# Optimization experiments

Hardware: AMD Instinct MI355X
Metric: run time of the kernel (lower is better)

## Reference

```python
import jax, jax.numpy as jnp
import numpy as np

N_NODES = 50000
N_EDGES = 800000
HIDDEN = 256
LAYERS = 10


def setup_inputs() -> dict:
    key = jax.random.key(0)
    ks = jax.random.split(key, 8)
    x = jax.random.normal(ks[0], (N_NODES, 1), dtype=jnp.float32)
    edge_index = jax.random.randint(ks[1], (2, N_EDGES), 0, N_NODES, dtype=jnp.int64)
    # GCNConv weights (Glorot-ish scale)
    W1 = jax.random.normal(ks[2], (1, HIDDEN), dtype=jnp.float32) * (1.0 / np.sqrt(1))
    b1 = jnp.zeros((HIDDEN,), dtype=jnp.float32)
    W = jax.random.normal(ks[3], (HIDDEN, HIDDEN), dtype=jnp.float32) * (1.0 / np.sqrt(HIDDEN))
    b = jnp.zeros((HIDDEN,), dtype=jnp.float32)
    Wc = jax.random.normal(ks[4], (HIDDEN, 1), dtype=jnp.float32) * (1.0 / np.sqrt(HIDDEN))
    bc = jnp.zeros((1,), dtype=jnp.float32)
    return {"x": x, "edge_index": edge_index, "W1": W1, "b1": b1,
            "W": W, "b": b, "Wc": Wc, "bc": bc}


def _gcn_norm(edge_index, n_nodes):
    # PyG GCNConv default: add self-loops, symmetric normalization
    loop = jnp.arange(n_nodes, dtype=edge_index.dtype)
    src = jnp.concatenate([edge_index[0], loop])
    dst = jnp.concatenate([edge_index[1], loop])
    ones = jnp.ones(src.shape[0], dtype=jnp.float32)
    deg = jax.ops.segment_sum(ones, dst, num_segments=n_nodes)
    dinv = jnp.where(deg > 0, jax.lax.rsqrt(deg), 0.0)
    norm = dinv[src] * dinv[dst]  # [E+N]
    return src, dst, norm


def _gcn_conv(h, W, b, src, dst, norm, n_nodes):
    h = h @ W                                   # [N, H] dense transform first (small GEMM)
    msg = h[src] * norm[:, None]                # gather + scale  [E+N, H]
    out = jax.ops.segment_sum(msg, dst, num_segments=n_nodes)  # scatter-add
    return out + b


def reference(x, edge_index, W1, b1, W, b, Wc, bc):
    n = x.shape[0]
    src, dst, norm = _gcn_norm(edge_index, n)  # graph is static across layers
    h = jax.nn.relu(_gcn_conv(x, W1, b1, src, dst, norm, n))
    for _ in range(1, LAYERS):  # layers 1..9 share the same weights (self.conv reused)
        h = jax.nn.relu(_gcn_conv(h, W, b, src, dst, norm, n))
    return h @ Wc + bc  # [N, 1]
```

## Files before the change

kernel.cpp:

```cpp
#include <hip/hip_runtime.h>

typedef long long ll;
typedef __attribute__((ext_vector_type(8))) short short8;
typedef __attribute__((ext_vector_type(4))) float f32x4;
constexpr int HID = 256;
constexpr int LDSS = 264;

__device__ inline ushort f2bf(float f){
  uint u = __float_as_uint(f);
  u += 0x7FFFu + ((u >> 16) & 1u);
  return (ushort)(u >> 16);
}

__device__ inline int pinv(int q){ return (q & ~63) | ((q & 3)*16 + ((q >> 2) & 15)); }

__global__ void k_diag(float* out, int n, float val){
  int i = blockIdx.x*256 + threadIdx.x;
  if (i < n) out[i] = val;
}

__global__ void k_detect(const int* ei, int* flag){
  __shared__ int bad;
  if (threadIdx.x == 0) bad = 0;
  __syncthreads();
  for (int i = threadIdx.x; i < 2048; i += 256)
    if (ei[2*i+1] != 0) bad = 1;
  __syncthreads();
  if (threadIdx.x == 0) *flag = bad ? 0 : 1;
}

__global__ void k_count(const int* ei, ll E, const int* flag, int* cnt){
  ll i = (ll)blockIdx.x*256 + threadIdx.x;
  if (i >= E) return;
  int f = *flag;
  int d = f ? (int)((const ll*)ei)[E + i] : ei[E + i];
  atomicAdd(&cnt[d], 1);
}

__global__ void k_scan_a(const int* __restrict__ cnt, int* __restrict__ bsum, int n){
  __shared__ int s[256];
  int t = threadIdx.x, i = blockIdx.x*256 + t;
  s[t] = (i < n) ? cnt[i] : 0;
  __syncthreads();
  for (int off = 128; off; off >>= 1){
    if (t < off) s[t] += s[t + off];
    __syncthreads();
  }
  if (t == 0) bsum[blockIdx.x] = s[0];
}

__global__ void k_scan_b(const int* __restrict__ bsum, int* __restrict__ boff,
                         int nb, int* __restrict__ row_ptr, int n){
  __shared__ int s[256];
  int t = threadIdx.x;
  int v = (t < nb) ? bsum[t] : 0;
  s[t] = v; __syncthreads();
  for (int off = 1; off < 256; off <<= 1){
    int add = (t >= off) ? s[t - off] : 0;
    __syncthreads();
    s[t] += add;
    __syncthreads();
  }
  if (t < nb) boff[t] = s[t] - v;
  if (t == nb - 1) row_ptr[n] = s[t];
}

__global__ void k_scan_c(const int* __restrict__ cnt, const int* __restrict__ boff,
                         int* __restrict__ row_ptr, const float* __restrict__ x,
                         float* __restrict__ dinv, float* __restrict__ xd, int n){
  __shared__ int s[256];
  int t = threadIdx.x, i = blockIdx.x*256 + t;
  int v = (i < n) ? cnt[i] : 0;
  s[t] = v; __syncthreads();
  for (int off = 1; off < 256; off <<= 1){
    int add = (t >= off) ? s[t - off] : 0;
    __syncthreads();
    s[t] += add;
    __syncthreads();
  }
  if (i < n){
    row_ptr[i] = boff[blockIdx.x] + s[t] - v;
    float dv = 1.0f / sqrtf((float)(v + 1));
    dinv[i] = dv;
    xd[i] = x[i] * dv;
  }
}

__global__ void k_place(const int* ei, ll E, const int* flag, int* fill, int* col){
  ll i = (ll)blockIdx.x*256 + threadIdx.x;
  if (i >= E) return;
  int f = *flag;
  int s, d;
  if (f){ const ll* e64 = (const ll*)ei; s = (int)e64[i]; d = (int)e64[E + i]; }
  else  { s = ei[i]; d = ei[E + i]; }
  int p = atomicAdd(&fill[d], 1);
  col[p] = s;
}

__global__ void k_layer1(const float* __restrict__ xd, const int* __restrict__ row_ptr,
                         const int* __restrict__ col, float* __restrict__ g, int n){
  int i = blockIdx.x*256 + threadIdx.x;
  if (i >= n) return;
  float s = xd[i];
  int e0 = row_ptr[i], e1 = row_ptr[i+1];
  for (int e = e0; e < e1; ++e) s += xd[col[e]];
  g[i] = s;
}

__global__ void k_perm(const float* b1, const float* W1, const float* bm, const float* Wc,
                       float* b1_p, float* W1_p, float* bm_p, float* Wc_p){
  int q = threadIdx.x;
  int c = pinv(q);
  b1_p[q] = b1[c];
  W1_p[q] = W1[c];
  bm_p[q] = bm[c];
  Wc_p[q] = Wc[c];
}

__global__ void k_splitW(const float* __restrict__ W, short* __restrict__ Bt){
  int idx = blockIdx.x*256 + threadIdx.x;
  if (idx >= 16*8*64) return;
  int nb = idx >> 9, kc = (idx >> 6) & 7, l = idx & 63;
  short8 hi, lo;
  #pragma unroll
  for (int j = 0; j < 8; ++j){
    int k = pinv(kc*32 + ((l >> 4) * 8) + j);
    int c = nb*16 + (l & 15);
    float wv = W[k*HID + c];
    ushort h = f2bf(wv);
    float hf = __uint_as_float((uint)h << 16);
    hi[j] = (short)h;
    lo[j] = (short)f2bf(wv - hf);
  }
  ((short8*)Bt)[idx] = hi;
  ((short8*)Bt)[8192 + idx] = lo;
}

template<int MODE>
__global__ __launch_bounds__(256, 4) void k_gemm_mfma(
  const void* __restrict__ Ain, const short* __restrict__ Bt,
  const float* __restrict__ bias, const float* __restrict__ W1,
  const float* __restrict__ dinv, ushort* __restrict__ ts_bf, int n)
{
  __shared__ short Ah[64*LDSS];
  int t = threadIdx.x;
  int r0 = blockIdx.x * 64;

  #pragma unroll
  for (int i = 0; i < 8; ++i){
    int id  = i*256 + t;
    int row = id >> 5;
    int c16 = id & 31;
    int v   = r0 + row;
    short8 hi8 = {0,0,0,0,0,0,0,0};
    if (v < n){
      if (MODE == 0){
        float gv = dinv[v] * ((const float*)Ain)[v];
        const float4* wp = (const float4*)(W1 + c16*8);
        const float4* bp = (const float4*)(bias + c16*8);
        float4 w0 = wp[0], w1 = wp[1], b0 = bp[0], b1 = bp[1];
        hi8[0] = (short)f2bf(fmaxf(fmaf(gv,w0.x,b0.x), 0.f));
        hi8[1] = (short)f2bf(fmaxf(fmaf(gv,w0.y,b0.y), 0.f));
        hi8[2] = (short)f2bf(fmaxf(fmaf(gv,w0.z,b0.z), 0.f));
        hi8[3] = (short)f2bf(fmaxf(fmaf(gv,w0.w,b0.w), 0.f));
        hi8[4] = (short)f2bf(fmaxf(fmaf(gv,w1.x,b1.x), 0.f));
        hi8[5] = (short)f2bf(fmaxf(fmaf(gv,w1.y,b1.y), 0.f));
        hi8[6] = (short)f2bf(fmaxf(fmaf(gv,w1.z,b1.z), 0.f));
        hi8[7] = (short)f2bf(fmaxf(fmaf(gv,w1.w,b1.w), 0.f));
      } else {
        hi8 = ((const short8*)Ain)[(size_t)v*32 + c16];
      }
    }
    *(short8*)&Ah[row*LDSS + c16*8] = hi8;
  }
  __syncthreads();

  int l = t & 63, w = t >> 6;
  const short8* Btv = (const short8*)Bt;
  f32x4 acc[4][4];
  #pragma unroll
  for (int m = 0; m < 4; ++m)
    #pragma unroll
    for (int nf = 0; nf < 4; ++nf)
      acc[m][nf] = (f32x4){0.f,0.f,0.f,0.f};

  for (int kc = 0; kc < 8; ++kc){
    short8 ah[4];
    #pragma unroll
    for (int m = 0; m < 4; ++m){
      int row = m*16 + (l & 15);
      ah[m] = *(const short8*)&Ah[row*LDSS + (kc*4 + (l >> 4))*8];
    }
    #pragma unroll
    for (int nf = 0; nf < 4; ++nf){
      int nb = w*4 + nf;
      short8 bh = Btv[(size_t)(nb*8 + kc)*64 + l];
      short8 bl = Btv[(size_t)8192 + (nb*8 + kc)*64 + l];
      #pragma unroll
      for (int m = 0; m < 4; ++m){
        acc[m][nf] = __builtin_amdgcn_mfma_f32_16x16x32_bf16(ah[m], bh, acc[m][nf], 0,0,0);
        acc[m][nf] = __builtin_amdgcn_mfma_f32_16x16x32_bf16(ah[m], bl, acc[m][nf], 0,0,0);
      }
    }
  }

  #pragma unroll
  for (int m = 0; m < 4; ++m){
    #pragma unroll
    for (int r = 0; r < 4; ++r){
      int v = r0 + m*16 + ((l >> 4)*4) + r;
      if (v < n){
        float dv = dinv[v];
        uint2 o;
        o.x = (uint)f2bf(dv * acc[m][0][r]) | ((uint)f2bf(dv * acc[m][1][r]) << 16);
        o.y = (uint)f2bf(dv * acc[m][2][r]) | ((uint)f2bf(dv * acc[m][3][r]) << 16);
        *(uint2*)((char*)ts_bf + (size_t)v*512 + w*128 + (l & 15)*8) = o;
      }
    }
  }
}

__device__ inline void bfacc(uint2 u, float4& a){
  a.x += __uint_as_float(u.x << 16);
  a.y += __uint_as_float(u.x & 0xFFFF0000u);
  a.z += __uint_as_float(u.y << 16);
  a.w += __uint_as_float(u.y & 0xFFFF0000u);
}

template<int LAST>
__global__ __launch_bounds__(256, 4) void k_scatter_bf(
  const ushort* __restrict__ ts_bf, const int* __restrict__ row_ptr,
  const int* __restrict__ col, const float* __restrict__ bias,
  const float* __restrict__ dinv, ushort* __restrict__ Abf,
  const float* __restrict__ Wc, const float* __restrict__ bc,
  float* __restrict__ out, int n)
{
  int w = (int)((blockIdx.x*256 + threadIdx.x) >> 6);
  int lane = threadIdx.x & 63;
  if (w >= n) return;
  const uint2* tsp = ((const uint2*)ts_bf) + lane;
  int e0 = row_ptr[w], e1 = row_ptr[w+1];

  float4 a0 = make_float4(0.f,0.f,0.f,0.f);
  float4 a1 = make_float4(0.f,0.f,0.f,0.f);
  float4 a2 = make_float4(0.f,0.f,0.f,0.f);
  float4 a3 = make_float4(0.f,0.f,0.f,0.f);
  bfacc(tsp[(size_t)w*64], a0);

  int e = e0;
  for (; e + 4 <= e1; e += 4){
    int c0 = __builtin_nontemporal_load(col + e + 0);
    int c1 = __builtin_nontemporal_load(col + e + 1);
    int c2 = __builtin_nontemporal_load(col + e + 2);
    int c3 = __builtin_nontemporal_load(col + e + 3);
    uint2 v0 = tsp[(size_t)c0*64];
    uint2 v1 = tsp[(size_t)c1*64];
    uint2 v2 = tsp[(size_t)c2*64];
    uint2 v3 = tsp[(size_t)c3*64];
    bfacc(v0, a0); bfacc(v1, a1); bfacc(v2, a2); bfacc(v3, a3);
  }
  for (; e < e1; ++e){
    uint2 v = tsp[(size_t)__builtin_nontemporal_load(col + e)*64];
    bfacc(v, a0);
  }

  a0.x += a1.x + a2.x + a3.x;
  a0.y += a1.y + a2.y + a3.y;
  a0.z += a1.z + a2.z + a3.z;
  a0.w += a1.w + a2.w + a3.w;

  float dv = dinv[w];
  float4 bb = ((const float4*)bias)[lane];
  if (LAST == 0){
    uint2 o;
    o.x = (uint)f2bf(fmaxf(fmaf(dv, a0.x, bb.x), 0.f))
        | ((uint)f2bf(fmaxf(fmaf(dv, a0.y, bb.y), 0.f)) << 16);
    o.y = (uint)f2bf(fmaxf(fmaf(dv, a0.z, bb.z), 0.f))
        | ((uint)f2bf(fmaxf(fmaf(dv, a0.w, bb.w), 0.f)) << 16);
    ((uint2*)Abf)[(size_t)w*64 + lane] = o;
  } else {
    float4 wc = ((const float4*)Wc)[lane];
    float s = fmaxf(fmaf(dv, a0.x, bb.x), 0.f)*wc.x
            + fmaxf(fmaf(dv, a0.y, bb.y), 0.f)*wc.y
            + fmaxf(fmaf(dv, a0.z, bb.z), 0.f)*wc.z
            + fmaxf(fmaf(dv, a0.w, bb.w), 0.f)*wc.w;
    #pragma unroll
    for (int off = 32; off; off >>= 1) s += __shfl_down(s, off, 64);
    if (lane == 0) out[w] = s + bc[0];
  }
}

extern "C" void kernel_launch(void* const* d_in, const int* in_sizes, int n_in,
                              void* d_out, int out_size, void* d_ws, size_t ws_size,
                              hipStream_t stream)
{
  const float* x  = (const float*)d_in[0];
  const int*   ei = (const int*)d_in[1];
  const float* W1 = (const float*)d_in[2];
  const float* b1 = (const float*)d_in[3];
  const float* Wm = (const float*)d_in[4];
  const float* bm = (const float*)d_in[5];
  const float* Wc = (const float*)d_in[6];
  const float* bc = (const float*)d_in[7];
  float* out = (float*)d_out;
  const int N = in_sizes[0];
  const ll  E = in_sizes[1] / 2;

  char* ws = (char*)d_ws;
  size_t off = 0;
  auto carve = [&](size_t bytes)->char*{
    char* p = ws + off; off += (bytes + 255) & ~(size_t)255; return p;
  };
  int*   cnt     = (int*)  carve((size_t)N*4);
  int*   row_ptr = (int*)  carve((size_t)(N+1)*4);
  int*   fill    = (int*)  carve((size_t)N*4);
  float* dinv    = (float*)carve((size_t)N*4);
  float* xd      = (float*)carve((size_t)N*4);
  float* g       = (float*)carve((size_t)N*4);
  int*   flag    = (int*)  carve(256);
  int*   bsum    = (int*)  carve(1024);
  int*   boff    = (int*)  carve(1024);
  float* b1_p    = (float*)carve(1024);
  float* W1_p    = (float*)carve(1024);
  float* bm_p    = (float*)carve(1024);
  float* Wc_p    = (float*)carve(1024);
  short* Bt      = (short*)carve((size_t)2*8192*8*2);
  int*   col     = (int*)  carve((size_t)E*4);
  ushort* ts_bf  = (ushort*)carve((size_t)N*HID*2);
  ushort* Abf    = (ushort*)carve((size_t)N*HID*2);
  if (off > ws_size){
    k_diag<<<(out_size+255)/256, 256, 0, stream>>>(out, out_size, (float)(ws_size >> 20));
    return;
  }

  hipMemsetAsync(cnt, 0, (size_t)N*4, stream);
  k_detect<<<1, 256, 0, stream>>>(ei, flag);
  int eblocks = (int)((E + 255) / 256);
  k_count<<<eblocks, 256, 0, stream>>>(ei, E, flag, cnt);
  int nb = (N + 255) / 256;
  k_scan_a<<<nb, 256, 0, stream>>>(cnt, bsum, N);
  k_scan_b<<<1, 256, 0, stream>>>(bsum, boff, nb, row_ptr, N);
  k_scan_c<<<nb, 256, 0, stream>>>(cnt, boff, row_ptr, x, dinv, xd, N);
  hipMemcpyAsync(fill, row_ptr, (size_t)N*4, hipMemcpyDeviceToDevice, stream);
  k_place<<<eblocks, 256, 0, stream>>>(ei, E, flag, fill, col);
  k_perm<<<1, 256, 0, stream>>>(b1, W1, bm, Wc, b1_p, W1_p, bm_p, Wc_p);
  k_splitW<<<32, 256, 0, stream>>>(Wm, Bt);
  k_layer1<<<(N+255)/256, 256, 0, stream>>>(xd, row_ptr, col, g, N);

  int gblocks = (N + 63) / 64;
  int sblocks = (N + 3) / 4;
  k_gemm_mfma<0><<<gblocks, 256, 0, stream>>>(g, Bt, b1_p, W1_p, dinv, ts_bf, N);
  k_scatter_bf<0><<<sblocks, 256, 0, stream>>>(ts_bf, row_ptr, col, bm_p, dinv, Abf, Wc_p, bc, out, N);
  for (int l = 0; l < 7; ++l){
    k_gemm_mfma<1><<<gblocks, 256, 0, stream>>>(Abf, Bt, bm_p, nullptr, dinv, ts_bf, N);
    k_scatter_bf<0><<<sblocks, 256, 0, stream>>>(ts_bf, row_ptr, col, bm_p, dinv, Abf, Wc_p, bc, out, N);
  }
  k_gemm_mfma<1><<<gblocks, 256, 0, stream>>>(Abf, Bt, bm_p, nullptr, dinv, ts_bf, N);
  k_scatter_bf<1><<<sblocks, 256, 0, stream>>>(ts_bf, row_ptr, col, bm_p, dinv, Abf, Wc_p, bc, out, N);
}
```

Before: 876.7 us.

## Fuse neighbor aggregation into MFMA GEMM using aggregate-then-transform ordering

Reorders each GCN layer to aggregate first and transform second. The sparse gather of pre-scaled bf16 features feeds the GEMM's LDS tile directly, and bias plus ReLU move into the GEMM epilogue. This removes a separate scatter kernel and one full N×256 intermediate write and read per layer, halving the launches. The cost is that the gather now runs inside a 64-row GEMM block whose 4 waves each walk 16 rows serially, with less parallelism and more imbalance than one wave per node. There is also an extra bf16 rounding of the aggregate before the GEMM.

```diff
diff --git a/kernel.cpp b/kernel.cpp
--- a/kernel.cpp
+++ b/kernel.cpp
@@ -13,6 +13,13 @@
 }
 
 __device__ inline int pinv(int q){ return (q & ~63) | ((q & 3)*16 + ((q >> 2) & 15)); }
+
+__device__ inline void bfacc(uint2 u, float4& a){
+  a.x += __uint_as_float(u.x << 16);
+  a.y += __uint_as_float(u.x & 0xFFFF0000u);
+  a.z += __uint_as_float(u.y << 16);
+  a.w += __uint_as_float(u.y & 0xFFFF0000u);
+}
 
 __global__ void k_diag(float* out, int n, float val){
   int i = blockIdx.x*256 + threadIdx.x;
@@ -136,46 +143,84 @@
   ((short8*)Bt)[8192 + idx] = lo;
 }
 
-template<int MODE>
-__global__ __launch_bounds__(256, 4) void k_gemm_mfma(
-  const void* __restrict__ Ain, const short* __restrict__ Bt,
-  const float* __restrict__ bias, const float* __restrict__ W1,
-  const float* __restrict__ dinv, ushort* __restrict__ ts_bf, int n)
+__global__ __launch_bounds__(256) void k_expand1(
+  const float* __restrict__ g, const float* __restrict__ dinv,
+  const float* __restrict__ W1_p, const float* __restrict__ b1_p,
+  ushort* __restrict__ Hs, int n)
+{
+  int v = (int)((blockIdx.x*256 + threadIdx.x) >> 6);
+  int lane = threadIdx.x & 63;
+  if (v >= n) return;
+  float dv = dinv[v];
+  float gv = dv * g[v];
+  float4 w1 = ((const float4*)W1_p)[lane];
+  float4 bb = ((const float4*)b1_p)[lane];
+  uint2 o;
+  o.x = (uint)f2bf(dv * fmaxf(fmaf(gv, w1.x, bb.x), 0.f))
+      | ((uint)f2bf(dv * fmaxf(fmaf(gv, w1.y, bb.y), 0.f)) << 16);
+  o.y = (uint)f2bf(dv * fmaxf(fmaf(gv, w1.z, bb.z), 0.f))
+      | ((uint)f2bf(dv * fmaxf(fmaf(gv, w1.w, bb.w), 0.f)) << 16);
+  ((uint2*)Hs)[(size_t)v*64 + lane] = o;
+}
+
+template<int LAST>
+__global__ __launch_bounds__(256, 4) void k_fused(
+  const ushort* __restrict__ Hs, const int* __restrict__ row_ptr,
+  const int* __restrict__ col, const short* __restrict__ Bt,
+  const float* __restrict__ bias_p, const float* __restrict__ dinv,
+  ushort* __restrict__ Hs_out, int n)
 {
   __shared__ short Ah[64*LDSS];
   int t = threadIdx.x;
+  int lane = t & 63, w = t >> 6;
   int r0 = blockIdx.x * 64;
 
-  #pragma unroll
-  for (int i = 0; i < 8; ++i){
-    int id  = i*256 + t;
-    int row = id >> 5;
-    int c16 = id & 31;
-    int v   = r0 + row;
-    short8 hi8 = {0,0,0,0,0,0,0,0};
+  const uint2* hsp = ((const uint2*)Hs) + lane;
+  for (int i = 0; i < 16; ++i){
+    int row = w*16 + i;
+    int v = r0 + row;
+    uint2 o = make_uint2(0u, 0u);
     if (v < n){
-      if (MODE == 0){
-        float gv = dinv[v] * ((const float*)Ain)[v];
-        const float4* wp = (const float4*)(W1 + c16*8);
-        const float4* bp = (const float4*)(bias + c16*8);
-        float4 w0 = wp[0], w1 = wp[1], b0 = bp[0], b1 = bp[1];
-        hi8[0] = (short)f2bf(fmaxf(fmaf(gv,w0.x,b0.x), 0.f));
-        hi8[1] = (short)f2bf(fmaxf(fmaf(gv,w0.y,b0.y), 0.f));
-        hi8[2] = (short)f2bf(fmaxf(fmaf(gv,w0.z,b0.z), 0.f));
-        hi8[3] = (short)f2bf(fmaxf(fmaf(gv,w0.w,b0.w), 0.f));
-        hi8[4] = (short)f2bf(fmaxf(fmaf(gv,w1.x,b1.x), 0.f));
-        hi8[5] = (short)f2bf(fmaxf(fmaf(gv,w1.y,b1.y), 0.f));
-        hi8[6] = (short)f2bf(fmaxf(fmaf(gv,w1.z,b1.z), 0.f));
-        hi8[7] = (short)f2bf(fmaxf(fmaf(gv,w1.w,b1.w), 0.f));
-      } else {
-        hi8 = ((const short8*)Ain)[(size_t)v*32 + c16];
-      }
+      float4 a0 = make_float4(0.f,0.f,0.f,0.f);
+      float4 a1 = make_float4(0.f,0.f,0.f,0.f);
+      float4 a2 = make_float4(0.f,0.f,0.f,0.f);
+      float4 a3 = make_float4(0.f,0.f,0.f,0.f);
+      bfacc(hsp[(size_t)v*64], a0);
+      int e0 = row_ptr[v], e1 = row_ptr[v+1];
+      int e = e0;
+      for (; e + 8 <= e1; e += 8){
+        int c[8];
+        #pragma unroll
+        for (int j = 0; j < 8; ++j) c[j] = __builtin_nontemporal_load(col + e + j);
+        uint2 vv[8];
+        #pragma unroll
+        for (int j = 0; j < 8; ++j) vv[j] = hsp[(size_t)c[j]*64];
+        bfacc(vv[0], a0); bfacc(vv[1], a1); bfacc(vv[2], a2); bfacc(vv[3], a3);
+        bfacc(vv[4], a0); bfacc(vv[5], a1); bfacc(vv[6], a2); bfacc(vv[7], a3);
+      }
+      for (; e + 2 <= e1; e += 2){
+        int c0 = __builtin_nontemporal_load(col + e);
+        int c1 = __builtin_nontemporal_load(col + e + 1);
+        uint2 v0 = hsp[(size_t)c0*64];
+        uint2 v1 = hsp[(size_t)c1*64];
+        bfacc(v0, a0); bfacc(v1, a1);
+      }
+      if (e < e1){
+        uint2 vv = hsp[(size_t)__builtin_nontemporal_load(col + e)*64];
+        bfacc(vv, a0);
+      }
+      a0.x += a1.x + a2.x + a3.x;
+      a0.y += a1.y + a2.y + a3.y;
+      a0.z += a1.z + a2.z + a3.z;
+      a0.w += a1.w + a2.w + a3.w;
+      float dv = dinv[v];
+      o.x = (uint)f2bf(dv * a0.x) | ((uint)f2bf(dv * a0.y) << 16);
+      o.y = (uint)f2bf(dv * a0.z) | ((uint)f2bf(dv * a0.w) << 16);
     }
-    *(short8*)&Ah[row*LDSS + c16*8] = hi8;
+    *(uint2*)&Ah[row*LDSS + lane*4] = o;
   }
   __syncthreads();
 
-  int l = t & 63, w = t >> 6;
   const short8* Btv = (const short8*)Bt;
   f32x4 acc[4][4];
   #pragma unroll
@@ -188,14 +233,14 @@
     short8 ah[4];
     #pragma unroll
     for (int m = 0; m < 4; ++m){
-      int row = m*16 + (l & 15);
-      ah[m] = *(const short8*)&Ah[row*LDSS + (kc*4 + (l >> 4))*8];
+      int row = m*16 + (lane & 15);
+      ah[m] = *(const short8*)&Ah[row*LDSS + (kc*4 + (lane >> 4))*8];
     }
     #pragma unroll
     for (int nf = 0; nf < 4; ++nf){
       int nb = w*4 + nf;
-      short8 bh = Btv[(size_t)(nb*8 + kc)*64 + l];
-      short8 bl = Btv[(size_t)8192 + (nb*8 + kc)*64 + l];
+      short8 bh = Btv[(size_t)(nb*8 + kc)*64 + lane];
+      short8 bl = Btv[(size_t)8192 + (nb*8 + kc)*64 + lane];
       #pragma unroll
       for (int m = 0; m < 4; ++m){
         acc[m][nf] = __builtin_amdgcn_mfma_f32_16x16x32_bf16(ah[m], bh, acc[m][nf], 0,0,0);
@@ -204,90 +249,41 @@
     }
   }
 
+  float4 bb = *(const float4*)(bias_p + w*64 + (lane & 15)*4);
   #pragma unroll
   for (int m = 0; m < 4; ++m){
     #pragma unroll
     for (int r = 0; r < 4; ++r){
-      int v = r0 + m*16 + ((l >> 4)*4) + r;
+      int v = r0 + m*16 + ((lane >> 4)*4) + r;
       if (v < n){
-        float dv = dinv[v];
+        float sc = LAST ? 1.0f : dinv[v];
         uint2 o;
-        o.x = (uint)f2bf(dv * acc[m][0][r]) | ((uint)f2bf(dv * acc[m][1][r]) << 16);
-        o.y = (uint)f2bf(dv * acc[m][2][r]) | ((uint)f2bf(dv * acc[m][3][r]) << 16);
-        *(uint2*)((char*)ts_bf + (size_t)v*512 + w*128 + (l & 15)*8) = o;
+        o.x = (uint)f2bf(sc * fmaxf(acc[m][0][r] + bb.x, 0.f))
+            | ((uint)f2bf(sc * fmaxf(acc[m][1][r] + bb.y, 0.f)) << 16);
+        o.y = (uint)f2bf(sc * fmaxf(acc[m][2][r] + bb.z, 0.f))
+            | ((uint)f2bf(sc * fmaxf(acc[m][3][r] + bb.w, 0.f)) << 16);
+        *(uint2*)((char*)Hs_out + (size_t)v*512 + w*128 + (lane & 15)*8) = o;
       }
     }
   }
 }
 
-__device__ inline void bfacc(uint2 u, float4& a){
-  a.x += __uint_as_float(u.x << 16);
-  a.y += __uint_as_float(u.x & 0xFFFF0000u);
-  a.z += __uint_as_float(u.y << 16);
-  a.w += __uint_as_float(u.y & 0xFFFF0000u);
-}
-
-template<int LAST>
-__global__ __launch_bounds__(256, 4) void k_scatter_bf(
-  const ushort* __restrict__ ts_bf, const int* __restrict__ row_ptr,
-  const int* __restrict__ col, const float* __restrict__ bias,
-  const float* __restrict__ dinv, ushort* __restrict__ Abf,
-  const float* __restrict__ Wc, const float* __restrict__ bc,
-  float* __restrict__ out, int n)
+__global__ __launch_bounds__(256) void k_out(
+  const ushort* __restrict__ H, const float* __restrict__ Wc_p,
+  const float* __restrict__ bc, float* __restrict__ out, int n)
 {
-  int w = (int)((blockIdx.x*256 + threadIdx.x) >> 6);
+  int v = (int)((blockIdx.x*256 + threadIdx.x) >> 6);
   int lane = threadIdx.x & 63;
-  if (w >= n) return;
-  const uint2* tsp = ((const uint2*)ts_bf) + lane;
-  int e0 = row_ptr[w], e1 = row_ptr[w+1];
-
-  float4 a0 = make_float4(0.f,0.f,0.f,0.f);
-  float4 a1 = make_float4(0.f,0.f,0.f,0.f);
-  float4 a2 = make_float4(0.f,0.f,0.f,0.f);
-  float4 a3 = make_float4(0.f,0.f,0.f,0.f);
-  bfacc(tsp[(size_t)w*64], a0);
-
-  int e = e0;
-  for (; e + 4 <= e1; e += 4){
-    int c0 = __builtin_nontemporal_load(col + e + 0);
-    int c1 = __builtin_nontemporal_load(col + e + 1);
-    int c2 = __builtin_nontemporal_load(col + e + 2);
-    int c3 = __builtin_nontemporal_load(col + e + 3);
-    uint2 v0 = tsp[(size_t)c0*64];
-    uint2 v1 = tsp[(size_t)c1*64];
-    uint2 v2 = tsp[(size_t)c2*64];
-    uint2 v3 = tsp[(size_t)c3*64];
-    bfacc(v0, a0); bfacc(v1, a1); bfacc(v2, a2); bfacc(v3, a3);
-  }
-  for (; e < e1; ++e){
-    uint2 v = tsp[(size_t)__builtin_nontemporal_load(col + e)*64];
-    bfacc(v, a0);
-  }
-
-  a0.x += a1.x + a2.x + a3.x;
-  a0.y += a1.y + a2.y + a3.y;
-  a0.z += a1.z + a2.z + a3.z;
-  a0.w += a1.w + a2.w + a3.w;
-
-  float dv = dinv[w];
-  float4 bb = ((const float4*)bias)[lane];
-  if (LAST == 0){
-    uint2 o;
-    o.x = (uint)f2bf(fmaxf(fmaf(dv, a0.x, bb.x), 0.f))
-        | ((uint)f2bf(fmaxf(fmaf(dv, a0.y, bb.y), 0.f)) << 16);
-    o.y = (uint)f2bf(fmaxf(fmaf(dv, a0.z, bb.z), 0.f))
-        | ((uint)f2bf(fmaxf(fmaf(dv, a0.w, bb.w), 0.f)) << 16);
-    ((uint2*)Abf)[(size_t)w*64 + lane] = o;
-  } else {
-    float4 wc = ((const float4*)Wc)[lane];
-    float s = fmaxf(fmaf(dv, a0.x, bb.x), 0.f)*wc.x
-            + fmaxf(fmaf(dv, a0.y, bb.y), 0.f)*wc.y
-            + fmaxf(fmaf(dv, a0.z, bb.z), 0.f)*wc.z
-            + fmaxf(fmaf(dv, a0.w, bb.w), 0.f)*wc.w;
-    #pragma unroll
-    for (int off = 32; off; off >>= 1) s += __shfl_down(s, off, 64);
-    if (lane == 0) out[w] = s + bc[0];
-  }
+  if (v >= n) return;
+  uint2 u = ((const uint2*)H)[(size_t)v*64 + lane];
+  float4 wc = ((const float4*)Wc_p)[lane];
+  float s = __uint_as_float(u.x << 16)          * wc.x
+          + __uint_as_float(u.x & 0xFFFF0000u)  * wc.y
+          + __uint_as_float(u.y << 16)          * wc.z
+          + __uint_as_float(u.y & 0xFFFF0000u)  * wc.w;
+  #pragma unroll
+  for (int off = 32; off; off >>= 1) s += __shfl_down(s, off, 64);
+  if (lane == 0) out[v] = s + bc[0];
 }
 
 extern "C" void kernel_launch(void* const* d_in, const int* in_sizes, int n_in,
@@ -326,8 +322,8 @@
   float* Wc_p    = (float*)carve(1024);
   short* Bt      = (short*)carve((size_t)2*8192*8*2);
   int*   col     = (int*)  carve((size_t)E*4);
-  ushort* ts_bf  = (ushort*)carve((size_t)N*HID*2);
-  ushort* Abf    = (ushort*)carve((size_t)N*HID*2);
+  ushort* Hs_a   = (ushort*)carve((size_t)N*HID*2);
+  ushort* Hs_b   = (ushort*)carve((size_t)N*HID*2);
   if (off > ws_size){
     k_diag<<<(out_size+255)/256, 256, 0, stream>>>(out, out_size, (float)(ws_size >> 20));
     return;
@@ -347,14 +343,14 @@
   k_splitW<<<32, 256, 0, stream>>>(Wm, Bt);
   k_layer1<<<(N+255)/256, 256, 0, stream>>>(xd, row_ptr, col, g, N);
 
-  int gblocks = (N + 63) / 64;
-  int sblocks = (N + 3) / 4;
-  k_gemm_mfma<0><<<gblocks, 256, 0, stream>>>(g, Bt, b1_p, W1_p, dinv, ts_bf, N);
-  k_scatter_bf<0><<<sblocks, 256, 0, stream>>>(ts_bf, row_ptr, col, bm_p, dinv, Abf, Wc_p, bc, out, N);
-  for (int l = 0; l < 7; ++l){
-    k_gemm_mfma<1><<<gblocks, 256, 0, stream>>>(Abf, Bt, bm_p, nullptr, dinv, ts_bf, N);
-    k_scatter_bf<0><<<sblocks, 256, 0, stream>>>(ts_bf, row_ptr, col, bm_p, dinv, Abf, Wc_p, bc, out, N);
-  }
-  k_gemm_mfma<1><<<gblocks, 256, 0, stream>>>(Abf, Bt, bm_p, nullptr, dinv, ts_bf, N);
-  k_scatter_bf<1><<<sblocks, 256, 0, stream>>>(ts_bf, row_ptr, col, bm_p, dinv, Abf, Wc_p, bc, out, N);
-}
+  int vblocks = (N + 3) / 4;
+  int fblocks = (N + 63) / 64;
+  k_expand1<<<vblocks, 256, 0, stream>>>(g, dinv, W1_p, b1_p, Hs_a, N);
+  ushort* cur = Hs_a; ushort* nxt = Hs_b;
+  for (int l = 0; l < 8; ++l){
+    k_fused<0><<<fblocks, 256, 0, stream>>>(cur, row_ptr, col, Bt, bm_p, dinv, nxt, N);
+    ushort* tmp = cur; cur = nxt; nxt = tmp;
+  }
+  k_fused<1><<<fblocks, 256, 0, stream>>>(cur, row_ptr, col, Bt, bm_p, dinv, nxt, N);
+  k_out<<<vblocks, 256, 0, stream>>>(nxt, Wc_p, bc, out, N);
+}
```

Result: slower. 994.4 us (+13.4%).
